# Optimization experiments

Hardware: AMD Instinct MI355X
Metric: run time of the kernel (lower is better)

The kernel has to match this reference:

```python
import jax, jax.numpy as jnp
import numpy as np

B, SQ, D, H = 2, 1024, 2048, 16
HD = D // H
SP, SS, SM = 1024, 1024, 512
DP, DS, DM = 1280, 1024, 768
INNER = 4 * D


def rms_norm(x, w, eps=1e-6):
    x32 = x.astype(jnp.float32)
    y = x32 * jax.lax.rsqrt(jnp.mean(x32 * x32, axis=-1, keepdims=True) + eps)
    return y.astype(x.dtype) * w


def layer_norm(x, g, b, eps=1e-5):
    mu = jnp.mean(x, axis=-1, keepdims=True)
    var = jnp.mean((x - mu) ** 2, axis=-1, keepdims=True)
    return (x - mu) * jax.lax.rsqrt(var + eps) * g + b


def setup_inputs() -> dict:
    key = jax.random.key(0)
    ks = jax.random.split(key, 32)
    s = lambda i, shape, sc=0.02: jax.random.normal(ks[i], shape, jnp.float32) * sc
    inp = {
        "query_states": jax.random.normal(ks[0], (B, SQ, D), jnp.float32),
        "protein_kv_states": jax.random.normal(ks[1], (B, SP, DP), jnp.float32),
        "structure_kv_states": jax.random.normal(ks[2], (B, SS, DS), jnp.float32),
        "msa_kv_states": jax.random.normal(ks[3], (B, SM, DM), jnp.float32),
        "query_attn_mask": jnp.ones((B, SQ), jnp.float32),
        "protein_kv_attn_mask": jnp.ones((B, SP), jnp.float32),
        "structure_kv_attn_mask": jnp.ones((B, SS), jnp.float32),
        "msa_kv_attn_mask": jnp.ones((B, SM), jnp.float32),
        "rms_w": jnp.ones((D,), jnp.float32),
        "Wq": s(4, (D, D)), "bq": jnp.zeros((D,), jnp.float32),
        "Wkp": s(5, (DP, D)), "bkp": jnp.zeros((D,), jnp.float32),
        "Wvp": s(6, (DP, D)), "bvp": jnp.zeros((D,), jnp.float32),
        "Wks": s(7, (DS, D)), "bks": jnp.zeros((D,), jnp.float32),
        "Wvs": s(8, (DS, D)), "bvs": jnp.zeros((D,), jnp.float32),
        "Wkm": s(9, (DM, D)), "bkm": jnp.zeros((D,), jnp.float32),
        "Wvm": s(10, (DM, D)), "bvm": jnp.zeros((D,), jnp.float32),
        "Wo": s(11, (D, D)), "bo": jnp.zeros((D,), jnp.float32),
        "ln_g": jnp.ones((D,), jnp.float32), "ln_b": jnp.zeros((D,), jnp.float32),
        "W1": s(12, (D, INNER)), "W2": s(13, (INNER, D)),
        "gate_attn": jax.random.normal(ks[14], (1,), jnp.float32) * 0.5,
        "gate_ffw": jax.random.normal(ks[15], (1,), jnp.float32) * 0.5,
    }
    return inp


def _forward(query_states, protein_kv_states, structure_kv_states, msa_kv_states,
             query_attn_mask, protein_kv_attn_mask, structure_kv_attn_mask, msa_kv_attn_mask,
             rms_w, Wq, bq, Wkp, bkp, Wvp, bvp, Wks, bks, Wvs, bvs, Wkm, bkm, Wvm, bvm,
             Wo, bo, ln_g, ln_b, W1, W2, gate_attn, gate_ffw):
    scale = jnp.float32(H) ** -0.5  # NOTE: original scales by num_heads, not head_dim
    kv_mask = jnp.concatenate([protein_kv_attn_mask, structure_kv_attn_mask, msa_kv_attn_mask], axis=1)  # [B, SKV]

    q = rms_norm(query_states, rms_w) @ Wq + bq                               # [B,SQ,D]
    k = jnp.concatenate([protein_kv_states @ Wkp + bkp,
                         structure_kv_states @ Wks + bks,
                         msa_kv_states @ Wkm + bkm], axis=1)                  # [B,SKV,D]
    v = jnp.concatenate([protein_kv_states @ Wvp + bvp,
                         structure_kv_states @ Wvs + bvs,
                         msa_kv_states @ Wvm + bvm], axis=1)

    def split_heads(x):  # [B,S,D] -> [B,H,S,HD]
        return x.reshape(x.shape[0], x.shape[1], H, HD).transpose(0, 2, 1, 3)

    qh = split_heads(q) * scale
    kh = split_heads(k)
    vh = split_heads(v)

    scores = jnp.einsum("bhqd,bhkd->bhqk", qh, kh)
    scores = scores - jax.lax.stop_gradient(jnp.max(scores, axis=-1, keepdims=True))
    attn_mask = query_attn_mask[:, None, :, None] * kv_mask[:, None, None, :]  # [B,1,SQ,SKV]
    scores = jnp.where(attn_mask == 0, jnp.finfo(scores.dtype).min, scores)
    probs = jax.nn.softmax(scores, axis=-1)
    ctx = jnp.einsum("bhqk,bhkd->bhqd", probs, vh)
    ctx = ctx.transpose(0, 2, 1, 3).reshape(B, SQ, D)
    attn_out = ctx @ Wo + bo

    h = query_states + jnp.tanh(gate_attn) * attn_out
    ff = jax.nn.gelu(layer_norm(h, ln_g, ln_b) @ W1, approximate=False) @ W2
    return h + ff * jnp.tanh(gate_ffw)


def reference(query_states, protein_kv_states, structure_kv_states, msa_kv_states,
              query_attn_mask, protein_kv_attn_mask, structure_kv_attn_mask, msa_kv_attn_mask,
              rms_w, Wq, bq, Wkp, bkp, Wvp, bvp, Wks, bks, Wvs, bvs, Wkm, bkm, Wvm, bvm,
              Wo, bo, ln_g, ln_b, W1, W2, gate_attn, gate_ffw):
    return _forward(query_states, protein_kv_states, structure_kv_states, msa_kv_states,
                    query_attn_mask, protein_kv_attn_mask, structure_kv_attn_mask, msa_kv_attn_mask,
                    rms_w, Wq, bq, Wkp, bkp, Wvp, bvp, Wks, bks, Wvs, bvs, Wkm, bkm, Wvm, bvm,
                    Wo, bo, ln_g, ln_b, W1, W2, gate_attn, gate_ffw)
```

## Files before the change

kernel.cpp:

```cpp
#include <hip/hip_runtime.h>
#include <math.h>

#define D_MODEL 2048
#define NHEAD 16
#define HDIM 128
#define SQL 1024
#define SKVL 2560

__global__ __launch_bounds__(256) void rms_kernel(
    const float* __restrict__ X, const float* __restrict__ w, float* __restrict__ Y)
{
    int row = blockIdx.x;
    const float4* x4 = (const float4*)(X + (size_t)row * D_MODEL);
    const float4* w4 = (const float4*)w;
    float4* y4 = (float4*)(Y + (size_t)row * D_MODEL);
    __shared__ float red[256];
    float s = 0.f;
    for (int i = threadIdx.x; i < D_MODEL / 4; i += 256) {
        float4 v = x4[i];
        s += v.x * v.x + v.y * v.y + v.z * v.z + v.w * v.w;
    }
    red[threadIdx.x] = s; __syncthreads();
    for (int st = 128; st > 0; st >>= 1) {
        if (threadIdx.x < st) red[threadIdx.x] += red[threadIdx.x + st];
        __syncthreads();
    }
    float r = rsqrtf(red[0] * (1.f / D_MODEL) + 1e-6f);
    for (int i = threadIdx.x; i < D_MODEL / 4; i += 256) {
        float4 v = x4[i], ww = w4[i];
        float4 o;
        o.x = v.x * r * ww.x; o.y = v.y * r * ww.y;
        o.z = v.z * r * ww.z; o.w = v.w * r * ww.w;
        y4[i] = o;
    }
}

__global__ __launch_bounds__(256) void ln_kernel(
    const float* __restrict__ X, const float* __restrict__ g, const float* __restrict__ b,
    float* __restrict__ Y)
{
    int row = blockIdx.x;
    const float4* x4 = (const float4*)(X + (size_t)row * D_MODEL);
    __shared__ float red[256];
    float s = 0.f;
    for (int i = threadIdx.x; i < D_MODEL / 4; i += 256) {
        float4 v = x4[i];
        s += v.x + v.y + v.z + v.w;
    }
    red[threadIdx.x] = s; __syncthreads();
    for (int st = 128; st > 0; st >>= 1) {
        if (threadIdx.x < st) red[threadIdx.x] += red[threadIdx.x + st];
        __syncthreads();
    }
    float mu = red[0] * (1.f / D_MODEL);
    __syncthreads();
    float vv = 0.f;
    for (int i = threadIdx.x; i < D_MODEL / 4; i += 256) {
        float4 v = x4[i];
        float a0 = v.x - mu, a1 = v.y - mu, a2 = v.z - mu, a3 = v.w - mu;
        vv += a0 * a0 + a1 * a1 + a2 * a2 + a3 * a3;
    }
    red[threadIdx.x] = vv; __syncthreads();
    for (int st = 128; st > 0; st >>= 1) {
        if (threadIdx.x < st) red[threadIdx.x] += red[threadIdx.x + st];
        __syncthreads();
    }
    float rstd = rsqrtf(red[0] * (1.f / D_MODEL) + 1e-5f);
    const float4* g4 = (const float4*)g;
    const float4* b4 = (const float4*)b;
    float4* y4 = (float4*)(Y + (size_t)row * D_MODEL);
    for (int i = threadIdx.x; i < D_MODEL / 4; i += 256) {
        float4 v = x4[i], gg = g4[i], bb = b4[i];
        float4 o;
        o.x = (v.x - mu) * rstd * gg.x + bb.x;
        o.y = (v.y - mu) * rstd * gg.y + bb.y;
        o.z = (v.z - mu) * rstd * gg.z + bb.z;
        o.w = (v.w - mu) * rstd * gg.w + bb.w;
        y4[i] = o;
    }
}

template <int EPI>
__global__ __launch_bounds__(256) void gemm_kernel(
    const float* __restrict__ A, const float* __restrict__ W,
    const float* __restrict__ bias, float* __restrict__ C,
    int M, int N, int K, int Sin, int Sout, int rowOff,
    const float* __restrict__ res, const float* __restrict__ gate)
{
    __shared__ float As[16][68];
    __shared__ float Bs[16][64];
    const int t = threadIdx.x;
    const int tq = t >> 4, tn = t & 15;
    const int bm = blockIdx.y * 64, bn = blockIdx.x * 64;
    const int am = t >> 2, ak4 = (t & 3) << 2;
    const int kb = t >> 4, nb4 = (t & 15) << 2;
    float acc[4][4] = {};
    for (int kt = 0; kt < K; kt += 16) {
        float4 a4 = *(const float4*)(A + (size_t)(bm + am) * K + kt + ak4);
        float4 b4 = *(const float4*)(W + (size_t)(kt + kb) * N + bn + nb4);
        As[ak4 + 0][am] = a4.x; As[ak4 + 1][am] = a4.y;
        As[ak4 + 2][am] = a4.z; As[ak4 + 3][am] = a4.w;
        *(float4*)&Bs[kb][nb4] = b4;
        __syncthreads();
#pragma unroll
        for (int k = 0; k < 16; ++k) {
            float4 av = *(const float4*)&As[k][tq << 2];
            float4 bv = *(const float4*)&Bs[k][tn << 2];
            float aa[4] = {av.x, av.y, av.z, av.w};
            float bb[4] = {bv.x, bv.y, bv.z, bv.w};
#pragma unroll
            for (int i = 0; i < 4; ++i)
#pragma unroll
                for (int j = 0; j < 4; ++j)
                    acc[i][j] = fmaf(aa[i], bb[j], acc[i][j]);
        }
        __syncthreads();
    }
    float tg = 0.f;
    if (EPI == 1 || EPI == 3) tg = tanhf(gate[0]);
#pragma unroll
    for (int i = 0; i < 4; ++i) {
        int r = bm + (tq << 2) + i;
        int orow = (r / Sin) * Sout + rowOff + (r % Sin);
        float vout[4];
#pragma unroll
        for (int j = 0; j < 4; ++j) {
            float v = acc[i][j];
            if (EPI == 0 || EPI == 1) v += bias[bn + (tn << 2) + j];
            if (EPI == 2) v = 0.5f * v * (1.f + erff(v * 0.70710678118654752f));
            vout[j] = v;
        }
        if (EPI == 1 || EPI == 3) {
            const float4 rv = *(const float4*)(res + (size_t)orow * N + bn + (tn << 2));
            vout[0] = rv.x + tg * vout[0];
            vout[1] = rv.y + tg * vout[1];
            vout[2] = rv.z + tg * vout[2];
            vout[3] = rv.w + tg * vout[3];
        }
        float4 o; o.x = vout[0]; o.y = vout[1]; o.z = vout[2]; o.w = vout[3];
        *(float4*)(C + (size_t)orow * N + bn + (tn << 2)) = o;
    }
}

__global__ __launch_bounds__(256) void attn_kernel(
    const float* __restrict__ Q, const float* __restrict__ K, const float* __restrict__ V,
    const float* __restrict__ mp, const float* __restrict__ ms, const float* __restrict__ mm,
    float* __restrict__ O)
{
    __shared__ float Qs[128][68];
    __shared__ float Ks[128][36];
    __shared__ float Vs[32][132];
    __shared__ float Ps[32][68];
    __shared__ float mk[32];
    const int t = threadIdx.x;
    const int b = blockIdx.y >> 4;
    const int h = blockIdx.y & 15;
    const int q0 = blockIdx.x * 64;
    {
        int qi = t & 63, d0 = t >> 6;
        const float* qp = Q + ((size_t)(b * SQL + q0 + qi)) * D_MODEL + h * HDIM;
#pragma unroll
        for (int i = 0; i < 32; ++i) {
            int d = d0 + (i << 2);
            Qs[d][qi] = qp[d] * 0.25f;
        }
    }
    const int tq = t >> 4, tn = t & 15;
    float m_r[4], l_r[4], o_acc[4][8];
#pragma unroll
    for (int i = 0; i < 4; ++i) {
        m_r[i] = -1e30f; l_r[i] = 0.f;
#pragma unroll
        for (int d = 0; d < 8; ++d) o_acc[i][d] = 0.f;
    }
    __syncthreads();

    for (int kv0 = 0; kv0 < SKVL; kv0 += 32) {
        {
            int ki = t & 31, d0 = t >> 5;
            const float* kp = K + ((size_t)(b * SKVL + kv0 + ki)) * D_MODEL + h * HDIM;
#pragma unroll
            for (int i = 0; i < 16; ++i) {
                int d = d0 + (i << 3);
                Ks[d][ki] = kp[d];
            }
        }
#pragma unroll
        for (int i = 0; i < 4; ++i) {
            int f4 = t + (i << 8);
            int vi = f4 >> 5, d4 = (f4 & 31) << 2;
            *(float4*)&Vs[vi][d4] =
                *(const float4*)(V + ((size_t)(b * SKVL + kv0 + vi)) * D_MODEL + h * HDIM + d4);
        }
        if (t < 32) {
            int kvg = kv0 + t;
            float mv;
            if (kvg < 1024) mv = mp[b * 1024 + kvg];
            else if (kvg < 2048) mv = ms[b * 1024 + (kvg - 1024)];
            else mv = mm[b * 512 + (kvg - 2048)];
            mk[t] = mv;
        }
        __syncthreads();
        float s[4][2] = {};
        for (int d = 0; d < 128; ++d) {
            float4 qv = *(const float4*)&Qs[d][tq << 2];
            float2 kv2 = *(const float2*)&Ks[d][tn << 1];
            float qa[4] = {qv.x, qv.y, qv.z, qv.w};
#pragma unroll
            for (int i = 0; i < 4; ++i) {
                s[i][0] = fmaf(qa[i], kv2.x, s[i][0]);
                s[i][1] = fmaf(qa[i], kv2.y, s[i][1]);
            }
        }
        float mk0 = mk[tn << 1], mk1 = mk[(tn << 1) + 1];
        float alpha[4];
#pragma unroll
        for (int i = 0; i < 4; ++i) {
            float s0 = (mk0 == 0.f) ? -1e30f : s[i][0];
            float s1 = (mk1 == 0.f) ? -1e30f : s[i][1];
            float mx = fmaxf(s0, s1);
#pragma unroll
            for (int off = 1; off < 16; off <<= 1) mx = fmaxf(mx, __shfl_xor(mx, off, 64));
            float mnew = fmaxf(m_r[i], mx);
            alpha[i] = expf(m_r[i] - mnew);
            float p0 = expf(s0 - mnew), p1 = expf(s1 - mnew);
            float ps = p0 + p1;
#pragma unroll
            for (int off = 1; off < 16; off <<= 1) ps += __shfl_xor(ps, off, 64);
            m_r[i] = mnew;
            l_r[i] = l_r[i] * alpha[i] + ps;
            Ps[tn << 1][(tq << 2) + i] = p0;
            Ps[(tn << 1) + 1][(tq << 2) + i] = p1;
        }
        __syncthreads();
#pragma unroll
        for (int i = 0; i < 4; ++i)
#pragma unroll
            for (int dd = 0; dd < 8; ++dd) o_acc[i][dd] *= alpha[i];
        for (int kv = 0; kv < 32; ++kv) {
            float4 pv = *(const float4*)&Ps[kv][tq << 2];
            float4 va = *(const float4*)&Vs[kv][tn << 3];
            float4 vb = *(const float4*)&Vs[kv][(tn << 3) + 4];
            float pa[4] = {pv.x, pv.y, pv.z, pv.w};
            float vaa[4] = {va.x, va.y, va.z, va.w};
            float vbb[4] = {vb.x, vb.y, vb.z, vb.w};
#pragma unroll
            for (int i = 0; i < 4; ++i)
#pragma unroll
                for (int dd = 0; dd < 4; ++dd) {
                    o_acc[i][dd]     = fmaf(pa[i], vaa[dd], o_acc[i][dd]);
                    o_acc[i][dd + 4] = fmaf(pa[i], vbb[dd], o_acc[i][dd + 4]);
                }
        }
        __syncthreads();
    }
#pragma unroll
    for (int i = 0; i < 4; ++i) {
        float inv = 1.f / l_r[i];
        float* op = O + ((size_t)(b * SQL + q0 + (tq << 2) + i)) * D_MODEL + h * HDIM + (tn << 3);
        float4 o1, o2;
        o1.x = o_acc[i][0] * inv; o1.y = o_acc[i][1] * inv;
        o1.z = o_acc[i][2] * inv; o1.w = o_acc[i][3] * inv;
        o2.x = o_acc[i][4] * inv; o2.y = o_acc[i][5] * inv;
        o2.z = o_acc[i][6] * inv; o2.w = o_acc[i][7] * inv;
        *(float4*)op = o1; *(float4*)(op + 4) = o2;
    }
}

extern "C" void kernel_launch(void* const* d_in, const int* in_sizes, int n_in,
                              void* d_out, int out_size, void* d_ws, size_t ws_size,
                              hipStream_t stream)
{
    (void)in_sizes; (void)n_in; (void)out_size; (void)ws_size;
    const float* qs   = (const float*)d_in[0];
    const float* pkv  = (const float*)d_in[1];
    const float* skvi = (const float*)d_in[2];
    const float* mkvi = (const float*)d_in[3];
    const float* mskp = (const float*)d_in[5];
    const float* msks = (const float*)d_in[6];
    const float* mskm = (const float*)d_in[7];
    const float* rmsw = (const float*)d_in[8];
    const float* Wq  = (const float*)d_in[9];  const float* bq  = (const float*)d_in[10];
    const float* Wkp = (const float*)d_in[11]; const float* bkp = (const float*)d_in[12];
    const float* Wvp = (const float*)d_in[13]; const float* bvp = (const float*)d_in[14];
    const float* Wks = (const float*)d_in[15]; const float* bks = (const float*)d_in[16];
    const float* Wvs = (const float*)d_in[17]; const float* bvs = (const float*)d_in[18];
    const float* Wkm = (const float*)d_in[19]; const float* bkm = (const float*)d_in[20];
    const float* Wvm = (const float*)d_in[21]; const float* bvm = (const float*)d_in[22];
    const float* Wo  = (const float*)d_in[23]; const float* bo  = (const float*)d_in[24];
    const float* lng = (const float*)d_in[25]; const float* lnb = (const float*)d_in[26];
    const float* W1  = (const float*)d_in[27]; const float* W2  = (const float*)d_in[28];
    const float* ga  = (const float*)d_in[29]; const float* gf  = (const float*)d_in[30];

    float* ws = (float*)d_ws;
    const size_t SZ_Q  = (size_t)2048 * 2048;
    const size_t SZ_KV = (size_t)2 * SKVL * D_MODEL;
    float* qn  = ws;
    float* qb  = ws + SZ_Q;
    float* kb  = ws + 2 * SZ_Q;
    float* vb  = kb + SZ_KV;
    float* hb  = vb + SZ_KV;
    float* ctx = qn;
    float* xln = qb;
    float* tb  = kb;

    dim3 blk(256);
    rms_kernel<<<2048, blk, 0, stream>>>(qs, rmsw, qn);
    gemm_kernel<0><<<dim3(32, 32), blk, 0, stream>>>(qn, Wq, bq, qb,
        2048, 2048, 2048, 2048, 2048, 0, nullptr, nullptr);
    gemm_kernel<0><<<dim3(32, 32), blk, 0, stream>>>(pkv, Wkp, bkp, kb,
        2048, 2048, 1280, 1024, SKVL, 0, nullptr, nullptr);
    gemm_kernel<0><<<dim3(32, 32), blk, 0, stream>>>(skvi, Wks, bks, kb,
        2048, 2048, 1024, 1024, SKVL, 1024, nullptr, nullptr);
    gemm_kernel<0><<<dim3(32, 16), blk, 0, stream>>>(mkvi, Wkm, bkm, kb,
        1024, 2048, 768, 512, SKVL, 2048, nullptr, nullptr);
    gemm_kernel<0><<<dim3(32, 32), blk, 0, stream>>>(pkv, Wvp, bvp, vb,
        2048, 2048, 1280, 1024, SKVL, 0, nullptr, nullptr);
    gemm_kernel<0><<<dim3(32, 32), blk, 0, stream>>>(skvi, Wvs, bvs, vb,
        2048, 2048, 1024, 1024, SKVL, 1024, nullptr, nullptr);
    gemm_kernel<0><<<dim3(32, 16), blk, 0, stream>>>(mkvi, Wvm, bvm, vb,
        1024, 2048, 768, 512, SKVL, 2048, nullptr, nullptr);
    attn_kernel<<<dim3(16, 32), blk, 0, stream>>>(qb, kb, vb, mskp, msks, mskm, ctx);
    gemm_kernel<1><<<dim3(32, 32), blk, 0, stream>>>(ctx, Wo, bo, hb,
        2048, 2048, 2048, 2048, 2048, 0, qs, ga);
    ln_kernel<<<2048, blk, 0, stream>>>(hb, lng, lnb, xln);
    gemm_kernel<2><<<dim3(128, 32), blk, 0, stream>>>(xln, W1, nullptr, tb,
        2048, 8192, 2048, 2048, 2048, 0, nullptr, nullptr);
    gemm_kernel<3><<<dim3(32, 32), blk, 0, stream>>>(tb, W2, nullptr, (float*)d_out,
        2048, 2048, 8192, 2048, 2048, 0, hb, gf);
}
```

Baseline: 3.987 ms.

## Replace FP32 SIMT GEMMs with split-bf16 three-pass MFMA GEMMs

Every linear projection now runs on bf16 MFMA instructions. Each fp32 operand is split into a high and a low bf16 part, and three MFMA products (hh, lh, hl) recover near-fp32 accuracy. Activations are split by the norm and attention kernels or by a new split kernel. Weights are transposed and split per column chunk into a small workspace buffer just before each GEMM, using global_load_lds for tile loads. This is meant to remove the cost of scalar FMA GEMMs, but it adds split and transpose passes plus many small launches, some with low block counts (for example a 2x16 grid for W2), and drops the lowest-order cross term.

New measurement: 5.132 ms. 28.7% more time.

```diff
diff --git a/kernel.cpp b/kernel.cpp
--- a/kernel.cpp
+++ b/kernel.cpp
@@ -2,21 +2,41 @@
 #include <math.h>
 
 #define D_MODEL 2048
-#define NHEAD 16
-#define HDIM 128
 #define SQL 1024
 #define SKVL 2560
+#define HDIM 128
+
+typedef __attribute__((ext_vector_type(8))) short bfrag;
+typedef __attribute__((ext_vector_type(4))) float f32x4;
+typedef __attribute__((ext_vector_type(4))) unsigned short us4;
+
+__device__ __forceinline__ unsigned short f2bf(float x) {
+    unsigned int u = __float_as_uint(x);
+    u += 0x7FFFu + ((u >> 16) & 1u);
+    return (unsigned short)(u >> 16);
+}
+__device__ __forceinline__ float bf2f(unsigned short h) {
+    return __uint_as_float(((unsigned int)h) << 16);
+}
+__device__ __forceinline__ void split2(float x, unsigned short& h, unsigned short& l) {
+    h = f2bf(x);
+    l = f2bf(x - bf2f(h));
+}
+__device__ __forceinline__ void load16(const void* g, void* l) {
+    __builtin_amdgcn_global_load_lds((const __attribute__((address_space(1))) unsigned int*)g,
+                                     (__attribute__((address_space(3))) unsigned int*)l, 16, 0, 0);
+}
 
 __global__ __launch_bounds__(256) void rms_kernel(
-    const float* __restrict__ X, const float* __restrict__ w, float* __restrict__ Y)
+    const float* __restrict__ X, const float* __restrict__ w,
+    unsigned short* __restrict__ H, unsigned short* __restrict__ L)
 {
     int row = blockIdx.x;
     const float4* x4 = (const float4*)(X + (size_t)row * D_MODEL);
     const float4* w4 = (const float4*)w;
-    float4* y4 = (float4*)(Y + (size_t)row * D_MODEL);
     __shared__ float red[256];
     float s = 0.f;
-    for (int i = threadIdx.x; i < D_MODEL / 4; i += 256) {
+    for (int i = threadIdx.x; i < 512; i += 256) {
         float4 v = x4[i];
         s += v.x * v.x + v.y * v.y + v.z * v.z + v.w * v.w;
     }
@@ -25,37 +45,36 @@
         if (threadIdx.x < st) red[threadIdx.x] += red[threadIdx.x + st];
         __syncthreads();
     }
-    float r = rsqrtf(red[0] * (1.f / D_MODEL) + 1e-6f);
-    for (int i = threadIdx.x; i < D_MODEL / 4; i += 256) {
+    float r = rsqrtf(red[0] * (1.f / 2048.f) + 1e-6f);
+    for (int i = threadIdx.x; i < 512; i += 256) {
         float4 v = x4[i], ww = w4[i];
-        float4 o;
-        o.x = v.x * r * ww.x; o.y = v.y * r * ww.y;
-        o.z = v.z * r * ww.z; o.w = v.w * r * ww.w;
-        y4[i] = o;
+        float y[4] = {v.x * r * ww.x, v.y * r * ww.y, v.z * r * ww.z, v.w * r * ww.w};
+        us4 hh, ll;
+#pragma unroll
+        for (int j = 0; j < 4; ++j) { unsigned short a, b2; split2(y[j], a, b2); hh[j] = a; ll[j] = b2; }
+        *(us4*)&H[(size_t)row * 2048 + i * 4] = hh;
+        *(us4*)&L[(size_t)row * 2048 + i * 4] = ll;
     }
 }
 
 __global__ __launch_bounds__(256) void ln_kernel(
     const float* __restrict__ X, const float* __restrict__ g, const float* __restrict__ b,
-    float* __restrict__ Y)
+    unsigned short* __restrict__ H, unsigned short* __restrict__ L)
 {
     int row = blockIdx.x;
     const float4* x4 = (const float4*)(X + (size_t)row * D_MODEL);
     __shared__ float red[256];
     float s = 0.f;
-    for (int i = threadIdx.x; i < D_MODEL / 4; i += 256) {
-        float4 v = x4[i];
-        s += v.x + v.y + v.z + v.w;
-    }
+    for (int i = threadIdx.x; i < 512; i += 256) { float4 v = x4[i]; s += v.x + v.y + v.z + v.w; }
     red[threadIdx.x] = s; __syncthreads();
     for (int st = 128; st > 0; st >>= 1) {
         if (threadIdx.x < st) red[threadIdx.x] += red[threadIdx.x + st];
         __syncthreads();
     }
-    float mu = red[0] * (1.f / D_MODEL);
+    float mu = red[0] * (1.f / 2048.f);
     __syncthreads();
     float vv = 0.f;
-    for (int i = threadIdx.x; i < D_MODEL / 4; i += 256) {
+    for (int i = threadIdx.x; i < 512; i += 256) {
         float4 v = x4[i];
         float a0 = v.x - mu, a1 = v.y - mu, a2 = v.z - mu, a3 = v.w - mu;
         vv += a0 * a0 + a1 * a1 + a2 * a2 + a3 * a3;
@@ -65,87 +84,152 @@
         if (threadIdx.x < st) red[threadIdx.x] += red[threadIdx.x + st];
         __syncthreads();
     }
-    float rstd = rsqrtf(red[0] * (1.f / D_MODEL) + 1e-5f);
+    float rstd = rsqrtf(red[0] * (1.f / 2048.f) + 1e-5f);
     const float4* g4 = (const float4*)g;
     const float4* b4 = (const float4*)b;
-    float4* y4 = (float4*)(Y + (size_t)row * D_MODEL);
-    for (int i = threadIdx.x; i < D_MODEL / 4; i += 256) {
+    for (int i = threadIdx.x; i < 512; i += 256) {
         float4 v = x4[i], gg = g4[i], bb = b4[i];
-        float4 o;
-        o.x = (v.x - mu) * rstd * gg.x + bb.x;
-        o.y = (v.y - mu) * rstd * gg.y + bb.y;
-        o.z = (v.z - mu) * rstd * gg.z + bb.z;
-        o.w = (v.w - mu) * rstd * gg.w + bb.w;
-        y4[i] = o;
-    }
+        float y[4] = {(v.x - mu) * rstd * gg.x + bb.x, (v.y - mu) * rstd * gg.y + bb.y,
+                      (v.z - mu) * rstd * gg.z + bb.z, (v.w - mu) * rstd * gg.w + bb.w};
+        us4 hh, ll;
+#pragma unroll
+        for (int j = 0; j < 4; ++j) { unsigned short a, b2; split2(y[j], a, b2); hh[j] = a; ll[j] = b2; }
+        *(us4*)&H[(size_t)row * 2048 + i * 4] = hh;
+        *(us4*)&L[(size_t)row * 2048 + i * 4] = ll;
+    }
+}
+
+__global__ __launch_bounds__(256) void csplit(
+    const float* __restrict__ X, unsigned short* __restrict__ H, unsigned short* __restrict__ L, int n4)
+{
+    int i = blockIdx.x * 256 + threadIdx.x;
+    if (i >= n4) return;
+    float4 v = ((const float4*)X)[i];
+    float y[4] = {v.x, v.y, v.z, v.w};
+    us4 hh, ll;
+#pragma unroll
+    for (int j = 0; j < 4; ++j) { unsigned short a, b2; split2(y[j], a, b2); hh[j] = a; ll[j] = b2; }
+    ((us4*)H)[i] = hh; ((us4*)L)[i] = ll;
+}
+
+__global__ __launch_bounds__(256) void tsplit(
+    const float* __restrict__ W, unsigned short* __restrict__ Th, unsigned short* __restrict__ Tl,
+    int K, int N, int n0)
+{
+    __shared__ float tile[32][33];
+    int bk = blockIdx.x * 32, bnl = blockIdx.y * 32;
+    int t = threadIdx.x;
+    int r = t >> 3, c4 = (t & 7) << 2;
+    float4 v = *(const float4*)&W[(size_t)(bk + r) * N + n0 + bnl + c4];
+    tile[r][c4 + 0] = v.x; tile[r][c4 + 1] = v.y; tile[r][c4 + 2] = v.z; tile[r][c4 + 3] = v.w;
+    __syncthreads();
+    us4 hh, ll;
+#pragma unroll
+    for (int j = 0; j < 4; ++j) {
+        float x = tile[c4 + j][r];
+        unsigned short a, b2; split2(x, a, b2);
+        hh[j] = a; ll[j] = b2;
+    }
+    *(us4*)&Th[(size_t)(bnl + r) * K + bk + c4] = hh;
+    *(us4*)&Tl[(size_t)(bnl + r) * K + bk + c4] = ll;
 }
 
 template <int EPI>
-__global__ __launch_bounds__(256) void gemm_kernel(
-    const float* __restrict__ A, const float* __restrict__ W,
-    const float* __restrict__ bias, float* __restrict__ C,
-    int M, int N, int K, int Sin, int Sout, int rowOff,
+__global__ __launch_bounds__(256) void gemm_bf3(
+    const unsigned short* __restrict__ Ah, const unsigned short* __restrict__ Al,
+    const unsigned short* __restrict__ Bh, const unsigned short* __restrict__ Bl,
+    const float* __restrict__ bias, float* __restrict__ Cf,
+    unsigned short* __restrict__ Ch, unsigned short* __restrict__ Cl,
+    int N, int K, int Sin, int Sout, int rowOff, int nOff,
     const float* __restrict__ res, const float* __restrict__ gate)
 {
-    __shared__ float As[16][68];
-    __shared__ float Bs[16][64];
+    __shared__ unsigned short As[2][4096];
+    __shared__ unsigned short Bs[2][4096];
     const int t = threadIdx.x;
-    const int tq = t >> 4, tn = t & 15;
-    const int bm = blockIdx.y * 64, bn = blockIdx.x * 64;
-    const int am = t >> 2, ak4 = (t & 3) << 2;
-    const int kb = t >> 4, nb4 = (t & 15) << 2;
-    float acc[4][4] = {};
-    for (int kt = 0; kt < K; kt += 16) {
-        float4 a4 = *(const float4*)(A + (size_t)(bm + am) * K + kt + ak4);
-        float4 b4 = *(const float4*)(W + (size_t)(kt + kb) * N + bn + nb4);
-        As[ak4 + 0][am] = a4.x; As[ak4 + 1][am] = a4.y;
-        As[ak4 + 2][am] = a4.z; As[ak4 + 3][am] = a4.w;
-        *(float4*)&Bs[kb][nb4] = b4;
-        __syncthreads();
-#pragma unroll
-        for (int k = 0; k < 16; ++k) {
-            float4 av = *(const float4*)&As[k][tq << 2];
-            float4 bv = *(const float4*)&Bs[k][tn << 2];
-            float aa[4] = {av.x, av.y, av.z, av.w};
-            float bb[4] = {bv.x, bv.y, bv.z, bv.w};
-#pragma unroll
-            for (int i = 0; i < 4; ++i)
-#pragma unroll
-                for (int j = 0; j < 4; ++j)
-                    acc[i][j] = fmaf(aa[i], bb[j], acc[i][j]);
-        }
-        __syncthreads();
-    }
+    const int lane = t & 63;
+    const int w = t >> 6, wr = w >> 1, wc = w & 1;
+    const int fr = lane & 15, fq = lane >> 4;
+    const int bm = blockIdx.y * 128, bn = blockIdx.x * 128;
+    const int row0 = t >> 2, k80 = (t & 3) << 3;
+    const int row1 = row0 + 64;
+
+    f32x4 acc[4][4];
+    f32x4 zz = {0.f, 0.f, 0.f, 0.f};
+#pragma unroll
+    for (int i = 0; i < 4; ++i)
+#pragma unroll
+        for (int j = 0; j < 4; ++j) acc[i][j] = zz;
+
+    for (int kt = 0; kt < K; kt += 32) {
+        load16(&Ah[(size_t)(bm + row0) * K + kt + k80], &As[0][(size_t)t * 8]);
+        load16(&Ah[(size_t)(bm + row1) * K + kt + k80], &As[0][(size_t)(t + 256) * 8]);
+        load16(&Al[(size_t)(bm + row0) * K + kt + k80], &As[1][(size_t)t * 8]);
+        load16(&Al[(size_t)(bm + row1) * K + kt + k80], &As[1][(size_t)(t + 256) * 8]);
+        load16(&Bh[(size_t)(bn + row0) * K + kt + k80], &Bs[0][(size_t)t * 8]);
+        load16(&Bh[(size_t)(bn + row1) * K + kt + k80], &Bs[0][(size_t)(t + 256) * 8]);
+        load16(&Bl[(size_t)(bn + row0) * K + kt + k80], &Bs[1][(size_t)t * 8]);
+        load16(&Bl[(size_t)(bn + row1) * K + kt + k80], &Bs[1][(size_t)(t + 256) * 8]);
+        __syncthreads();
+
+        bfrag a_h[4], a_l[4], b_h[4], b_l[4];
+#pragma unroll
+        for (int i = 0; i < 4; ++i) {
+            int ra = (wr * 64 + i * 16 + fr) * 32 + fq * 8;
+            a_h[i] = *(const bfrag*)&As[0][ra];
+            a_l[i] = *(const bfrag*)&As[1][ra];
+            int rb = (wc * 64 + i * 16 + fr) * 32 + fq * 8;
+            b_h[i] = *(const bfrag*)&Bs[0][rb];
+            b_l[i] = *(const bfrag*)&Bs[1][rb];
+        }
+#pragma unroll
+        for (int i = 0; i < 4; ++i)
+#pragma unroll
+            for (int j = 0; j < 4; ++j) {
+                acc[i][j] = __builtin_amdgcn_mfma_f32_16x16x32_bf16(a_h[i], b_h[j], acc[i][j], 0, 0, 0);
+                acc[i][j] = __builtin_amdgcn_mfma_f32_16x16x32_bf16(a_l[i], b_h[j], acc[i][j], 0, 0, 0);
+                acc[i][j] = __builtin_amdgcn_mfma_f32_16x16x32_bf16(a_h[i], b_l[j], acc[i][j], 0, 0, 0);
+            }
+        __syncthreads();
+    }
+
     float tg = 0.f;
     if (EPI == 1 || EPI == 3) tg = tanhf(gate[0]);
+    float bj[4] = {0.f, 0.f, 0.f, 0.f};
+    if (EPI == 0 || EPI == 1) {
+#pragma unroll
+        for (int j = 0; j < 4; ++j) bj[j] = bias[nOff + bn + wc * 64 + j * 16 + fr];
+    }
 #pragma unroll
     for (int i = 0; i < 4; ++i) {
-        int r = bm + (tq << 2) + i;
-        int orow = (r / Sin) * Sout + rowOff + (r % Sin);
-        float vout[4];
-#pragma unroll
-        for (int j = 0; j < 4; ++j) {
-            float v = acc[i][j];
-            if (EPI == 0 || EPI == 1) v += bias[bn + (tn << 2) + j];
-            if (EPI == 2) v = 0.5f * v * (1.f + erff(v * 0.70710678118654752f));
-            vout[j] = v;
-        }
-        if (EPI == 1 || EPI == 3) {
-            const float4 rv = *(const float4*)(res + (size_t)orow * N + bn + (tn << 2));
-            vout[0] = rv.x + tg * vout[0];
-            vout[1] = rv.y + tg * vout[1];
-            vout[2] = rv.z + tg * vout[2];
-            vout[3] = rv.w + tg * vout[3];
-        }
-        float4 o; o.x = vout[0]; o.y = vout[1]; o.z = vout[2]; o.w = vout[3];
-        *(float4*)(C + (size_t)orow * N + bn + (tn << 2)) = o;
+#pragma unroll
+        for (int r = 0; r < 4; ++r) {
+            int m = bm + wr * 64 + i * 16 + fq * 4 + r;
+            size_t orow = (EPI == 0) ? (size_t)((m / Sin) * Sout + rowOff + (m % Sin)) : (size_t)m;
+#pragma unroll
+            for (int j = 0; j < 4; ++j) {
+                int gn = nOff + bn + wc * 64 + j * 16 + fr;
+                float v = acc[i][j][r];
+                if (EPI == 0) {
+                    Cf[orow * N + gn] = v + bj[j];
+                } else if (EPI == 1) {
+                    v += bj[j];
+                    Cf[orow * N + gn] = res[orow * N + gn] + tg * v;
+                } else if (EPI == 2) {
+                    v = 0.5f * v * (1.f + erff(v * 0.70710678f));
+                    unsigned short a, b2; split2(v, a, b2);
+                    Ch[orow * N + gn] = a; Cl[orow * N + gn] = b2;
+                } else {
+                    Cf[orow * N + gn] = res[orow * N + gn] + tg * v;
+                }
+            }
+        }
     }
 }
 
 __global__ __launch_bounds__(256) void attn_kernel(
     const float* __restrict__ Q, const float* __restrict__ K, const float* __restrict__ V,
     const float* __restrict__ mp, const float* __restrict__ ms, const float* __restrict__ mm,
-    float* __restrict__ O)
+    unsigned short* __restrict__ CH, unsigned short* __restrict__ CL)
 {
     __shared__ float Qs[128][68];
     __shared__ float Ks[128][36];
@@ -257,13 +341,20 @@
 #pragma unroll
     for (int i = 0; i < 4; ++i) {
         float inv = 1.f / l_r[i];
-        float* op = O + ((size_t)(b * SQL + q0 + (tq << 2) + i)) * D_MODEL + h * HDIM + (tn << 3);
-        float4 o1, o2;
-        o1.x = o_acc[i][0] * inv; o1.y = o_acc[i][1] * inv;
-        o1.z = o_acc[i][2] * inv; o1.w = o_acc[i][3] * inv;
-        o2.x = o_acc[i][4] * inv; o2.y = o_acc[i][5] * inv;
-        o2.z = o_acc[i][6] * inv; o2.w = o_acc[i][7] * inv;
-        *(float4*)op = o1; *(float4*)(op + 4) = o2;
+        size_t bidx = ((size_t)(b * SQL + q0 + (tq << 2) + i)) * D_MODEL + h * HDIM + (tn << 3);
+        us4 h0, l0, h1, l1;
+#pragma unroll
+        for (int dd = 0; dd < 4; ++dd) {
+            unsigned short a, b2; split2(o_acc[i][dd] * inv, a, b2);
+            h0[dd] = a; l0[dd] = b2;
+        }
+#pragma unroll
+        for (int dd = 0; dd < 4; ++dd) {
+            unsigned short a, b2; split2(o_acc[i][dd + 4] * inv, a, b2);
+            h1[dd] = a; l1[dd] = b2;
+        }
+        *(us4*)&CH[bidx] = h0; *(us4*)&CH[bidx + 4] = h1;
+        *(us4*)&CL[bidx] = l0; *(us4*)&CL[bidx + 4] = l1;
     }
 }
 
@@ -292,40 +383,76 @@
     const float* W1  = (const float*)d_in[27]; const float* W2  = (const float*)d_in[28];
     const float* ga  = (const float*)d_in[29]; const float* gf  = (const float*)d_in[30];
 
-    float* ws = (float*)d_ws;
-    const size_t SZ_Q  = (size_t)2048 * 2048;
-    const size_t SZ_KV = (size_t)2 * SKVL * D_MODEL;
-    float* qn  = ws;
-    float* qb  = ws + SZ_Q;
-    float* kb  = ws + 2 * SZ_Q;
-    float* vb  = kb + SZ_KV;
-    float* hb  = vb + SZ_KV;
-    float* ctx = qn;
-    float* xln = qb;
-    float* tb  = kb;
+    char* base = (char*)d_ws;
+    unsigned short* pk_h = (unsigned short*)(base + 0);
+    unsigned short* pk_l = (unsigned short*)(base + 5242880);
+    unsigned short* sk_h = (unsigned short*)(base + 10485760);
+    unsigned short* sk_l = (unsigned short*)(base + 14680064);
+    unsigned short* mk_h = (unsigned short*)(base + 18874368);
+    unsigned short* mk_l = (unsigned short*)(base + 20447232);
+    unsigned short* wb_h = (unsigned short*)(base + 22020096);
+    unsigned short* wb_l = (unsigned short*)(base + 26214400);
+    float* qb = (float*)(base + 30408704);
+    float* kb = (float*)(base + 47185920);
+    float* vb = (float*)(base + 89128960);
+    unsigned short* qn_h = (unsigned short*)kb;
+    unsigned short* qn_l = (unsigned short*)((char*)kb + 8388608);
+    unsigned short* ctx_h = pk_h;
+    unsigned short* ctx_l = (unsigned short*)(base + 8388608);
+    unsigned short* xln_h = pk_h;
+    unsigned short* xln_l = (unsigned short*)(base + 8388608);
+    float* hb = qb;
+    unsigned short* tb_h = (unsigned short*)kb;
+    unsigned short* tb_l = (unsigned short*)((char*)kb + 33554432);
 
     dim3 blk(256);
-    rms_kernel<<<2048, blk, 0, stream>>>(qs, rmsw, qn);
-    gemm_kernel<0><<<dim3(32, 32), blk, 0, stream>>>(qn, Wq, bq, qb,
-        2048, 2048, 2048, 2048, 2048, 0, nullptr, nullptr);
-    gemm_kernel<0><<<dim3(32, 32), blk, 0, stream>>>(pkv, Wkp, bkp, kb,
-        2048, 2048, 1280, 1024, SKVL, 0, nullptr, nullptr);
-    gemm_kernel<0><<<dim3(32, 32), blk, 0, stream>>>(skvi, Wks, bks, kb,
-        2048, 2048, 1024, 1024, SKVL, 1024, nullptr, nullptr);
-    gemm_kernel<0><<<dim3(32, 16), blk, 0, stream>>>(mkvi, Wkm, bkm, kb,
-        1024, 2048, 768, 512, SKVL, 2048, nullptr, nullptr);
-    gemm_kernel<0><<<dim3(32, 32), blk, 0, stream>>>(pkv, Wvp, bvp, vb,
-        2048, 2048, 1280, 1024, SKVL, 0, nullptr, nullptr);
-    gemm_kernel<0><<<dim3(32, 32), blk, 0, stream>>>(skvi, Wvs, bvs, vb,
-        2048, 2048, 1024, 1024, SKVL, 1024, nullptr, nullptr);
-    gemm_kernel<0><<<dim3(32, 16), blk, 0, stream>>>(mkvi, Wvm, bvm, vb,
-        1024, 2048, 768, 512, SKVL, 2048, nullptr, nullptr);
-    attn_kernel<<<dim3(16, 32), blk, 0, stream>>>(qb, kb, vb, mskp, msks, mskm, ctx);
-    gemm_kernel<1><<<dim3(32, 32), blk, 0, stream>>>(ctx, Wo, bo, hb,
-        2048, 2048, 2048, 2048, 2048, 0, qs, ga);
-    ln_kernel<<<2048, blk, 0, stream>>>(hb, lng, lnb, xln);
-    gemm_kernel<2><<<dim3(128, 32), blk, 0, stream>>>(xln, W1, nullptr, tb,
-        2048, 8192, 2048, 2048, 2048, 0, nullptr, nullptr);
-    gemm_kernel<3><<<dim3(32, 32), blk, 0, stream>>>(tb, W2, nullptr, (float*)d_out,
-        2048, 2048, 8192, 2048, 2048, 0, hb, gf);
-}
+
+    rms_kernel<<<2048, blk, 0, stream>>>(qs, rmsw, qn_h, qn_l);
+    csplit<<<2560, blk, 0, stream>>>(pkv, pk_h, pk_l, 655360);
+    csplit<<<2048, blk, 0, stream>>>(skvi, sk_h, sk_l, 524288);
+    csplit<<<768,  blk, 0, stream>>>(mkvi, mk_h, mk_l, 196608);
+
+    auto proj = [&](const unsigned short* Ah, const unsigned short* Al,
+                    const float* W, const float* bias, float* out,
+                    int M, int K, int Nc, int nchunks, int Sin, int Sout, int rowOff) {
+        for (int c = 0; c < nchunks; ++c) {
+            tsplit<<<dim3(K / 32, Nc / 32), blk, 0, stream>>>(W, wb_h, wb_l, K, 2048, c * Nc);
+            gemm_bf3<0><<<dim3(Nc / 128, M / 128), blk, 0, stream>>>(
+                Ah, Al, wb_h, wb_l, bias, out, nullptr, nullptr,
+                2048, K, Sin, Sout, rowOff, c * Nc, nullptr, nullptr);
+        }
+    };
+
+    proj(qn_h, qn_l, Wq,  bq,  qb, 2048, 2048, 1024, 2, 2048, 2048, 0);
+    proj(pk_h, pk_l, Wkp, bkp, kb, 2048, 1280, 1024, 2, 1024, 2560, 0);
+    proj(sk_h, sk_l, Wks, bks, kb, 2048, 1024, 2048, 1, 1024, 2560, 1024);
+    proj(mk_h, mk_l, Wkm, bkm, kb, 1024, 768,  2048, 1, 512,  2560, 2048);
+    proj(pk_h, pk_l, Wvp, bvp, vb, 2048, 1280, 1024, 2, 1024, 2560, 0);
+    proj(sk_h, sk_l, Wvs, bvs, vb, 2048, 1024, 2048, 1, 1024, 2560, 1024);
+    proj(mk_h, mk_l, Wvm, bvm, vb, 1024, 768,  2048, 1, 512,  2560, 2048);
+
+    attn_kernel<<<dim3(16, 32), blk, 0, stream>>>(qb, kb, vb, mskp, msks, mskm, ctx_h, ctx_l);
+
+    for (int c = 0; c < 2; ++c) {
+        tsplit<<<dim3(64, 32), blk, 0, stream>>>(Wo, wb_h, wb_l, 2048, 2048, c * 1024);
+        gemm_bf3<1><<<dim3(8, 16), blk, 0, stream>>>(
+            ctx_h, ctx_l, wb_h, wb_l, bo, hb, nullptr, nullptr,
+            2048, 2048, 2048, 2048, 0, c * 1024, qs, ga);
+    }
+
+    ln_kernel<<<2048, blk, 0, stream>>>(hb, lng, lnb, xln_h, xln_l);
+
+    for (int c = 0; c < 8; ++c) {
+        tsplit<<<dim3(64, 32), blk, 0, stream>>>(W1, wb_h, wb_l, 2048, 8192, c * 1024);
+        gemm_bf3<2><<<dim3(8, 16), blk, 0, stream>>>(
+            xln_h, xln_l, wb_h, wb_l, nullptr, nullptr, tb_h, tb_l,
+            8192, 2048, 2048, 2048, 0, c * 1024, nullptr, nullptr);
+    }
+
+    for (int c = 0; c < 8; ++c) {
+        tsplit<<<dim3(256, 8), blk, 0, stream>>>(W2, wb_h, wb_l, 8192, 2048, c * 256);
+        gemm_bf3<3><<<dim3(2, 16), blk, 0, stream>>>(
+            tb_h, tb_l, wb_h, wb_l, nullptr, (float*)d_out, nullptr, nullptr,
+            2048, 8192, 2048, 2048, 0, c * 256, hb, gf);
+    }
+}
```
